# Optimization experiments

Measured on AMD Instinct MI355X. Metric: run time of the kernel, lower is better.

The kernel has to match this reference:

```python
import jax, jax.numpy as jnp
import numpy as np

ALPHA = 1.702
LIMIT = 7.0
EPS = 1e-5
TOP_K = 4


def setup_inputs() -> dict:
    key = jax.random.key(0)
    ks = jax.random.split(key, 8)
    B, S, H, I, E = 2, 512, 2048, 2048, 16
    return {
        "x": jax.random.normal(ks[0], (B, S, H), jnp.float32),
        "norm_w": jnp.ones((H,), jnp.float32),
        "gate_w": jax.random.normal(ks[1], (E, H), jnp.float32) * 0.02,
        "gate_b": jax.random.normal(ks[2], (E,), jnp.float32) * 0.02,
        "w1": jax.random.normal(ks[3], (E, 2 * I, H), jnp.float32) * 0.02,
        "b1": jax.random.normal(ks[4], (E, 2 * I), jnp.float32) * 0.02,
        "w2": jax.random.normal(ks[5], (E, H, I), jnp.float32) * 0.02,
        "b2": jax.random.normal(ks[6], (E, H), jnp.float32) * 0.02,
    }


def reference(x, norm_w, gate_w, gate_b, w1, b1, w2, b2):
    B, S, H = x.shape
    M = B * S
    E = gate_w.shape[0]
    xf = x.reshape(M, H)
    # RMSNorm
    t = xf * jax.lax.rsqrt(jnp.mean(xf * xf, axis=-1, keepdims=True) + EPS) * norm_w
    # Router: top-k over logits, then softmax over the selected k (sm_first=False)
    logits = t @ gate_w.T + gate_b  # [M, E]
    vals, idx = jax.lax.top_k(logits, TOP_K)
    gates_k = jax.nn.softmax(vals, axis=-1)  # [M, k]
    # Scatter top-k gate weights into dense [M, E] combine matrix
    G = jnp.zeros((M, E), x.dtype).at[jnp.arange(M)[:, None], idx].set(gates_k)
    # Expert MLP1 (all experts, combined sparsely below): [E, M, 2I]
    h = jnp.einsum('mh,eoh->emo', t, w1) + b1[:, None, :]
    # SwiGLU with clamp (gpt-oss): interleaved gate/linear columns
    a = jnp.minimum(h[..., ::2], LIMIT)
    b = jnp.clip(h[..., 1::2], -LIMIT, LIMIT)
    act = a * jax.nn.sigmoid(ALPHA * a) * (b + 1.0)  # [E, M, I]
    # Expert MLP2: [E, M, H]
    y = jnp.einsum('emi,edi->emd', act, w2) + b2[:, None, :]
    # Combine with gate weights (gammas scale full per-expert output incl. bias)
    delta = jnp.einsum('me,emd->md', G, y)
    return x + delta.reshape(B, S, H)
```

## Files before the change

kernel.cpp:

```cpp
#include <hip/hip_runtime.h>
#include <hip/hip_bf16.h>

constexpr int MTOK = 1024;
constexpr int HDIM = 2048;
constexpr int IDIM = 2048;
constexpr int NEXP = 16;
constexpr int TOPK = 4;
constexpr int NA   = MTOK * TOPK;

#define ALPHA_C 1.702f
#define LIMIT_C 7.0f
#define RMS_EPS 1e-5f

using short8 = __attribute__((ext_vector_type(8))) short;
using f32x4  = __attribute__((ext_vector_type(4))) float;

__device__ __forceinline__ unsigned short f2bf(float f) {
    unsigned u = __builtin_bit_cast(unsigned, f);
    u += 0x7fffu + ((u >> 16) & 1u);
    return (unsigned short)(u >> 16);
}

__device__ __forceinline__ unsigned pack2bf(float lo, float hi) {
    return (unsigned)f2bf(lo) | ((unsigned)f2bf(hi) << 16);
}

__device__ __forceinline__ short8 cvt8(const float4 a, const float4 b) {
    union { short8 s; unsigned u[4]; } r;
    r.u[0] = pack2bf(a.x, a.y);
    r.u[1] = pack2bf(a.z, a.w);
    r.u[2] = pack2bf(b.x, b.y);
    r.u[3] = pack2bf(b.z, b.w);
    return r.s;
}

__global__ __launch_bounds__(256) void k_router(
    const float* __restrict__ x, const float* __restrict__ norm_w,
    const float* __restrict__ gate_w, const float* __restrict__ gate_b,
    unsigned short* __restrict__ t_bf,
    int* __restrict__ counts, int* __restrict__ idx_of,
    int* __restrict__ slot_of, float* __restrict__ gate_mk)
{
    __shared__ float t_lds[HDIM];
    __shared__ float red[4];
    __shared__ float logits[NEXP];

    const int m   = blockIdx.x;
    const int tid = threadIdx.x;
    const float* xr = x + (size_t)m * HDIM;

    float4 v0 = ((const float4*)xr)[tid * 2];
    float4 v1 = ((const float4*)xr)[tid * 2 + 1];
    float ss = v0.x*v0.x + v0.y*v0.y + v0.z*v0.z + v0.w*v0.w
             + v1.x*v1.x + v1.y*v1.y + v1.z*v1.z + v1.w*v1.w;
    #pragma unroll
    for (int off = 32; off > 0; off >>= 1) ss += __shfl_down(ss, off);
    if ((tid & 63) == 0) red[tid >> 6] = ss;
    __syncthreads();
    float tot = red[0] + red[1] + red[2] + red[3];
    float scale = rsqrtf(tot / (float)HDIM + RMS_EPS);

    float4 n0 = ((const float4*)norm_w)[tid * 2];
    float4 n1 = ((const float4*)norm_w)[tid * 2 + 1];
    float t[8];
    t[0]=v0.x*scale*n0.x; t[1]=v0.y*scale*n0.y; t[2]=v0.z*scale*n0.z; t[3]=v0.w*scale*n0.w;
    t[4]=v1.x*scale*n1.x; t[5]=v1.y*scale*n1.y; t[6]=v1.z*scale*n1.z; t[7]=v1.w*scale*n1.w;
    short8 pk;
    #pragma unroll
    for (int j = 0; j < 8; ++j) {
        t_lds[tid * 8 + j] = t[j];
        pk[j] = (short)f2bf(t[j]);
    }
    *(short8*)(t_bf + (size_t)m * HDIM + tid * 8) = pk;
    __syncthreads();

    const int e = tid >> 4, j = tid & 15;
    const float4* gw4 = (const float4*)(gate_w + (size_t)e * HDIM);
    const float4* tl4 = (const float4*)t_lds;
    float part = 0.f;
    for (int h4 = j; h4 < HDIM / 4; h4 += 16) {
        float4 g = gw4[h4], tv = tl4[h4];
        part += g.x*tv.x + g.y*tv.y + g.z*tv.z + g.w*tv.w;
    }
    #pragma unroll
    for (int off = 8; off > 0; off >>= 1) part += __shfl_xor(part, off);
    if (j == 0) logits[e] = part + gate_b[e];
    __syncthreads();

    if (tid == 0) {
        float lv[NEXP];
        #pragma unroll
        for (int q = 0; q < NEXP; ++q) lv[q] = logits[q];
        int   sel[TOPK];
        float sv[TOPK];
        #pragma unroll
        for (int k = 0; k < TOPK; ++k) {
            float best = -1e30f; int bi = 0;
            for (int q = 0; q < NEXP; ++q)
                if (lv[q] > best) { best = lv[q]; bi = q; }
            sel[k] = bi; sv[k] = best; lv[bi] = -1e30f;
        }
        float mx = sv[0], s = 0.f, g[TOPK];
        #pragma unroll
        for (int k = 0; k < TOPK; ++k) { g[k] = __expf(sv[k] - mx); s += g[k]; }
        float inv = 1.f / s;
        #pragma unroll
        for (int k = 0; k < TOPK; ++k) {
            int a = m * TOPK + k;
            int slot = atomicAdd(&counts[sel[k]], 1);
            idx_of[a]  = sel[k];
            slot_of[a] = slot;
            gate_mk[a] = g[k] * inv;
        }
    }
}

__global__ void k_remap(const int* __restrict__ idx_of, const int* __restrict__ slot_of,
                        const int* __restrict__ counts,
                        int* __restrict__ token_of, int* __restrict__ rowidx)
{
    int a = blockIdx.x * blockDim.x + threadIdx.x;
    if (a >= NA) return;
    int e = idx_of[a];
    int off = 0;
    for (int q = 0; q < NEXP; ++q) off += (q < e) ? counts[q] : 0;
    int r = off + slot_of[a];
    token_of[r] = a >> 2;
    rowidx[a]   = r;
}

__global__ __launch_bounds__(256) void k_gemm1(
    const unsigned short* __restrict__ t_bf,
    const float* __restrict__ w1, const float* __restrict__ b1,
    const int* __restrict__ counts, const int* __restrict__ token_of,
    unsigned short* __restrict__ act)
{
    __shared__ unsigned char lB[2][2][5120];

    const int e = blockIdx.z;
    int ne = 0, roff = 0;
    #pragma unroll
    for (int q = 0; q < NEXP; ++q) {
        int cq = counts[q];
        roff += (q < e) ? cq : 0;
        ne    = (q == e) ? cq : ne;
    }
    const int brow = blockIdx.y * 320;
    if (brow >= ne) return;
    const int i0 = blockIdx.x * 32;
    const int tid = threadIdx.x;

    const int wv = tid >> 6, ln = tid & 63;
    const int lr = ln & 15, lk = ln >> 4;
    const int br = tid >> 2, bp = tid & 3;

    const unsigned short* aptr[5];
    #pragma unroll
    for (int mf = 0; mf < 5; ++mf) {
        int rg = brow + wv * 80 + mf * 16 + lr;
        int tok = token_of[roff + (rg < ne ? rg : 0)];
        aptr[mf] = t_bf + (size_t)tok * HDIM + lk * 8;
    }
    const int o = (br < 32) ? (2 * (i0 + br)) : (2 * (i0 + br - 32) + 1);
    const float* bsrc = w1 + ((size_t)e * (2 * IDIM) + o) * HDIM + bp * 16;

    float4 bS0[4], bS1[4], bS2[4], bS3[4];
    short8 aA0[5], aA1[5];
    f32x4  acc[5][4] = {};

    constexpr int NT = 32;

    {
        float4 p0 = *(const float4*)(bsrc);
        float4 p1 = *(const float4*)(bsrc + 4);
        float4 p2 = *(const float4*)(bsrc + 8);
        float4 p3 = *(const float4*)(bsrc + 12);
        *(short8*)(&lB[0][bp >> 1][br * 80 + (bp & 1) * 32])      = cvt8(p0, p1);
        *(short8*)(&lB[0][bp >> 1][br * 80 + (bp & 1) * 32 + 16]) = cvt8(p2, p3);
    }
    #pragma unroll
    for (int j = 0; j < 4; ++j) {
        bS1[j] = *(const float4*)(bsrc + 64  + j * 4);
        bS2[j] = *(const float4*)(bsrc + 128 + j * 4);
        bS3[j] = *(const float4*)(bsrc + 192 + j * 4);
    }
    #pragma unroll
    for (int mf = 0; mf < 5; ++mf) {
        aA0[mf] = *(const short8*)(aptr[mf]);
        aA1[mf] = *(const short8*)(aptr[mf] + 32);
    }
    asm volatile("s_waitcnt lgkmcnt(0)" ::: "memory");
    __builtin_amdgcn_s_barrier();

#define GSTEP(T_, SPUB, SISS)                                                            \
    {                                                                                    \
        const int t_ = (T_);                                                             \
        const int c_ = t_ & 1;                                                           \
        if (t_ + 1 < NT) {                                         \
            *(short8*)(&lB[c_ ^ 1][bp >> 1][br * 80 + (bp & 1) * 32])      =             \
                cvt8(SPUB[0], SPUB[1]);                                                  \
            *(short8*)(&lB[c_ ^ 1][bp >> 1][br * 80 + (bp & 1) * 32 + 16]) =             \
                cvt8(SPUB[2], SPUB[3]);                                                  \
        }                                                                                \
        if (t_ + 3 < NT) {                                           \
            _Pragma("unroll")                                                            \
            for (int j = 0; j < 4; ++j)                                                  \
                SISS[j] = *(const float4*)(bsrc + (t_ + 3) * 64 + j * 4);                \
        }                                                                                \
        short8 bfr[4];                                                                   \
        _Pragma("unroll")                                                                \
        for (int n = 0; n < 4; ++n)                                                      \
            bfr[n] = *(const short8*)(&lB[c_][0][(n * 16 + lr) * 80 + lk * 16]);         \
        _Pragma("unroll")                                                                \
        for (int mf = 0; mf < 5; ++mf)                                                   \
            _Pragma("unroll")                                                            \
            for (int n = 0; n < 4; ++n)                                                  \
                acc[mf][n] = __builtin_amdgcn_mfma_f32_16x16x32_bf16(                    \
                    aA0[mf], bfr[n], acc[mf][n], 0, 0, 0);                               \
        _Pragma("unroll")                                                                \
        for (int n = 0; n < 4; ++n)                                                      \
            bfr[n] = *(const short8*)(&lB[c_][1][(n * 16 + lr) * 80 + lk * 16]);         \
        _Pragma("unroll")                                                                \
        for (int mf = 0; mf < 5; ++mf)                                                   \
            _Pragma("unroll")                                                            \
            for (int n = 0; n < 4; ++n)                                                  \
                acc[mf][n] = __builtin_amdgcn_mfma_f32_16x16x32_bf16(                    \
                    aA1[mf], bfr[n], acc[mf][n], 0, 0, 0);                               \
        if (t_ + 1 < NT) {                           \
            _Pragma("unroll")                                                            \
            for (int mf = 0; mf < 5; ++mf) {                                             \
                aA0[mf] = *(const short8*)(aptr[mf] + (t_ + 1) * 64);                    \
                aA1[mf] = *(const short8*)(aptr[mf] + (t_ + 1) * 64 + 32);               \
            }                                                                            \
        }                                                                                \
        asm volatile("s_waitcnt lgkmcnt(0)" ::: "memory");                               \
        __builtin_amdgcn_s_barrier();                                                    \
    }

    for (int t8 = 0; t8 < NT / 4; ++t8) {
        const int tb = t8 * 4;
        GSTEP(tb + 0, bS1, bS3)
        GSTEP(tb + 1, bS2, bS0)
        GSTEP(tb + 2, bS3, bS1)
        GSTEP(tb + 3, bS0, bS2)
    }
#undef GSTEP

    #pragma unroll
    for (int n = 0; n < 2; ++n) {
        const int i = i0 + n * 16 + lr;
        const float ba = b1[(size_t)e * (2 * IDIM) + 2 * i];
        const float bb = b1[(size_t)e * (2 * IDIM) + 2 * i + 1];
        #pragma unroll
        for (int mf = 0; mf < 5; ++mf) {
            #pragma unroll
            for (int r = 0; r < 4; ++r) {
                const int rg = brow + wv * 80 + mf * 16 + lk * 4 + r;
                if (rg < ne) {
                    float ha = acc[mf][n][r] + ba;
                    float hb = acc[mf][n + 2][r] + bb;
                    float a = fminf(ha, LIMIT_C);
                    float b = fminf(fmaxf(hb, -LIMIT_C), LIMIT_C);
                    float s = 1.f / (1.f + __expf(-ALPHA_C * a));
                    act[(size_t)(roff + rg) * IDIM + i] = f2bf(a * s * (b + 1.f));
                }
            }
        }
    }
}

__global__ __launch_bounds__(256) void k_gemm2(
    const unsigned short* __restrict__ act,
    const float* __restrict__ w2, const float* __restrict__ b2,
    const int* __restrict__ counts, const int* __restrict__ token_of,
    unsigned short* __restrict__ ybuf)
{
    __shared__ unsigned char lB[2][2][5120];

    const int e = blockIdx.z;
    int ne = 0, roff = 0;
    #pragma unroll
    for (int q = 0; q < NEXP; ++q) {
        int cq = counts[q];
        roff += (q < e) ? cq : 0;
        ne    = (q == e) ? cq : ne;
    }
    const int brow = blockIdx.y * 320;
    if (brow >= ne) return;
    const int d0 = blockIdx.x * 64;
    const int tid = threadIdx.x;

    const int wv = tid >> 6, ln = tid & 63;
    const int lr = ln & 15, lk = ln >> 4;
    const int br = tid >> 2, bp = tid & 3;

    const unsigned short* aptr[5];
    #pragma unroll
    for (int mf = 0; mf < 5; ++mf) {
        int rg = brow + wv * 80 + mf * 16 + lr;
        int rc = (rg < ne) ? rg : 0;
        aptr[mf] = act + (size_t)(roff + rc) * IDIM + lk * 8;
    }
    const float* bsrc = w2 + ((size_t)e * HDIM + d0 + br) * IDIM + bp * 16;

    float4 bS0[4], bS1[4], bS2[4], bS3[4];
    short8 aA0[5], aA1[5];
    f32x4  acc[5][4] = {};

    constexpr int NT = 32;

    {
        float4 p0 = *(const float4*)(bsrc);
        float4 p1 = *(const float4*)(bsrc + 4);
        float4 p2 = *(const float4*)(bsrc + 8);
        float4 p3 = *(const float4*)(bsrc + 12);
        *(short8*)(&lB[0][bp >> 1][br * 80 + (bp & 1) * 32])      = cvt8(p0, p1);
        *(short8*)(&lB[0][bp >> 1][br * 80 + (bp & 1) * 32 + 16]) = cvt8(p2, p3);
    }
    #pragma unroll
    for (int j = 0; j < 4; ++j) {
        bS1[j] = *(const float4*)(bsrc + 64  + j * 4);
        bS2[j] = *(const float4*)(bsrc + 128 + j * 4);
        bS3[j] = *(const float4*)(bsrc + 192 + j * 4);
    }
    #pragma unroll
    for (int mf = 0; mf < 5; ++mf) {
        aA0[mf] = *(const short8*)(aptr[mf]);
        aA1[mf] = *(const short8*)(aptr[mf] + 32);
    }
    asm volatile("s_waitcnt lgkmcnt(0)" ::: "memory");
    __builtin_amdgcn_s_barrier();

#define GSTEP(T_, SPUB, SISS)                                                            \
    {                                                                                    \
        const int t_ = (T_);                                                             \
        const int c_ = t_ & 1;                                                           \
        if (t_ + 1 < NT) {                                                               \
            *(short8*)(&lB[c_ ^ 1][bp >> 1][br * 80 + (bp & 1) * 32])      =             \
                cvt8(SPUB[0], SPUB[1]);                                                  \
            *(short8*)(&lB[c_ ^ 1][bp >> 1][br * 80 + (bp & 1) * 32 + 16]) =             \
                cvt8(SPUB[2], SPUB[3]);                                                  \
        }                                                                                \
        if (t_ + 3 < NT) {                                                               \
            _Pragma("unroll")                                                            \
            for (int j = 0; j < 4; ++j)                                                  \
                SISS[j] = *(const float4*)(bsrc + (t_ + 3) * 64 + j * 4);                \
        }                                                                                \
        short8 bfr[4];                                                                   \
        _Pragma("unroll")                                                                \
        for (int n = 0; n < 4; ++n)                                                      \
            bfr[n] = *(const short8*)(&lB[c_][0][(n * 16 + lr) * 80 + lk * 16]);         \
        _Pragma("unroll")                                                                \
        for (int mf = 0; mf < 5; ++mf)                                                   \
            _Pragma("unroll")                                                            \
            for (int n = 0; n < 4; ++n)                                                  \
                acc[mf][n] = __builtin_amdgcn_mfma_f32_16x16x32_bf16(                    \
                    aA0[mf], bfr[n], acc[mf][n], 0, 0, 0);                               \
        _Pragma("unroll")                                                                \
        for (int n = 0; n < 4; ++n)                                                      \
            bfr[n] = *(const short8*)(&lB[c_][1][(n * 16 + lr) * 80 + lk * 16]);         \
        _Pragma("unroll")                                                                \
        for (int mf = 0; mf < 5; ++mf)                                                   \
            _Pragma("unroll")                                                            \
            for (int n = 0; n < 4; ++n)                                                  \
                acc[mf][n] = __builtin_amdgcn_mfma_f32_16x16x32_bf16(                    \
                    aA1[mf], bfr[n], acc[mf][n], 0, 0, 0);                               \
        if (t_ + 1 < NT) {                                                               \
            _Pragma("unroll")                                                            \
            for (int mf = 0; mf < 5; ++mf) {                                             \
                aA0[mf] = *(const short8*)(aptr[mf] + (t_ + 1) * 64);                    \
                aA1[mf] = *(const short8*)(aptr[mf] + (t_ + 1) * 64 + 32);               \
            }                                                                            \
        }                                                                                \
        asm volatile("s_waitcnt lgkmcnt(0)" ::: "memory");                               \
        __builtin_amdgcn_s_barrier();                                                    \
    }

    for (int t8 = 0; t8 < NT / 4; ++t8) {
        const int tb = t8 * 4;
        GSTEP(tb + 0, bS1, bS3)
        GSTEP(tb + 1, bS2, bS0)
        GSTEP(tb + 2, bS3, bS1)
        GSTEP(tb + 3, bS0, bS2)
    }
#undef GSTEP

    #pragma unroll
    for (int mf = 0; mf < 5; ++mf) {
        #pragma unroll
        for (int r = 0; r < 4; ++r) {
            const int rg = brow + wv * 80 + mf * 16 + lk * 4 + r;
            if (rg >= ne) continue;
            unsigned short* yrow = ybuf + (size_t)(roff + rg) * HDIM;
            #pragma unroll
            for (int n = 0; n < 4; ++n) {
                const int d = d0 + n * 16 + lr;
                yrow[d] = f2bf(acc[mf][n][r] + b2[(size_t)e * HDIM + d]);
            }
        }
    }
}

__global__ __launch_bounds__(256) void k_comb(
    const float* __restrict__ x, const unsigned short* __restrict__ ybuf,
    const int* __restrict__ rowidx, const float* __restrict__ gate_mk,
    float* __restrict__ out)
{
    __shared__ int   rws[TOPK];
    __shared__ float gws[TOPK];
    const int m = blockIdx.x;
    const int tid = threadIdx.x;
    if (tid < TOPK) {
        rws[tid] = rowidx[m * TOPK + tid];
        gws[tid] = gate_mk[m * TOPK + tid];
    }
    __syncthreads();
    const int d = tid * 8;
    float4 o0 = ((const float4*)(x + (size_t)m * HDIM + d))[0];
    float4 o1 = ((const float4*)(x + (size_t)m * HDIM + d))[1];
    #pragma unroll
    for (int k = 0; k < TOPK; ++k) {
        const float g = gws[k];
        short8 y = *(const short8*)(ybuf + (size_t)rws[k] * HDIM + d);
        float yv[8];
        #pragma unroll
        for (int j = 0; j < 8; ++j) {
            unsigned u = ((unsigned)(unsigned short)y[j]) << 16;
            yv[j] = __builtin_bit_cast(float, u);
        }
        o0.x += g * yv[0]; o0.y += g * yv[1]; o0.z += g * yv[2]; o0.w += g * yv[3];
        o1.x += g * yv[4]; o1.y += g * yv[5]; o1.z += g * yv[6]; o1.w += g * yv[7];
    }
    ((float4*)(out + (size_t)m * HDIM + d))[0] = o0;
    ((float4*)(out + (size_t)m * HDIM + d))[1] = o1;
}

extern "C" void kernel_launch(void* const* d_in, const int* in_sizes, int n_in,
                              void* d_out, int out_size, void* d_ws, size_t ws_size,
                              hipStream_t stream) {
    const float* x      = (const float*)d_in[0];
    const float* norm_w = (const float*)d_in[1];
    const float* gate_w = (const float*)d_in[2];
    const float* gate_b = (const float*)d_in[3];
    const float* w1     = (const float*)d_in[4];
    const float* b1     = (const float*)d_in[5];
    const float* w2     = (const float*)d_in[6];
    const float* b2     = (const float*)d_in[7];
    float* out = (float*)d_out;

    char* ws = (char*)d_ws;
    size_t off = 0;
    unsigned short* t_bf = (unsigned short*)(ws + off); off += (size_t)MTOK * HDIM * 2;
    unsigned short* actb = (unsigned short*)(ws + off); off += (size_t)NA * IDIM * 2;
    unsigned short* ybuf = (unsigned short*)(ws + off); off += (size_t)NA * HDIM * 2;
    int*   counts   = (int*)(ws + off);   off += 256;
    int*   idx_of   = (int*)(ws + off);   off += (size_t)NA * 4;
    int*   slot_of  = (int*)(ws + off);   off += (size_t)NA * 4;
    float* gate_mk  = (float*)(ws + off); off += (size_t)NA * 4;
    int*   token_of = (int*)(ws + off);   off += (size_t)NA * 4;
    int*   rowidx   = (int*)(ws + off);   off += (size_t)NA * 4;

    (void)hipMemsetAsync(counts, 0, 256, stream);
    k_router<<<MTOK, 256, 0, stream>>>(x, norm_w, gate_w, gate_b, t_bf,
                                       counts, idx_of, slot_of, gate_mk);
    k_remap<<<NA / 256, 256, 0, stream>>>(idx_of, slot_of, counts,
                                          token_of, rowidx);
    k_gemm1<<<dim3(IDIM / 32, (MTOK + 319) / 320, NEXP), 256, 0, stream>>>(
        t_bf, w1, b1, counts, token_of, actb);
    k_gemm2<<<dim3(HDIM / 64, (MTOK + 319) / 320, NEXP), 256, 0, stream>>>(
        actb, w2, b2, counts, token_of, ybuf);
    k_comb<<<MTOK, 256, 0, stream>>>(x, ybuf, rowidx, gate_mk, out);
}
```

Before: 428.4 us.

## Halve K-step in expert GEMMs to cut registers and target two blocks per CU

Both expert GEMM kernels move from 64-wide to 32-wide K steps (64 iterations instead of 32). This halves the staged B-fragment registers and the LDS tile, and the A fragments are now double-buffered in ping-pong register sets loaded one step ahead. Launch bounds now request two blocks per CU, and a sched_barrier pins global prefetches ahead of the LDS store and MFMA work. The aim is higher occupancy and better latency hiding, at the cost of twice as many barriers and smaller per-step MFMA batches.

```diff
diff --git a/kernel.cpp b/kernel.cpp
--- a/kernel.cpp
+++ b/kernel.cpp
@@ -129,13 +129,13 @@
     rowidx[a]   = r;
 }
 
-__global__ __launch_bounds__(256) void k_gemm1(
+__global__ __launch_bounds__(256, 2) void k_gemm1(
     const unsigned short* __restrict__ t_bf,
     const float* __restrict__ w1, const float* __restrict__ b1,
     const int* __restrict__ counts, const int* __restrict__ token_of,
     unsigned short* __restrict__ act)
 {
-    __shared__ unsigned char lB[2][2][5120];
+    __shared__ unsigned char lB[2][5120];
 
     const int e = blockIdx.z;
     int ne = 0, roff = 0;
@@ -162,87 +162,61 @@
         aptr[mf] = t_bf + (size_t)tok * HDIM + lk * 8;
     }
     const int o = (br < 32) ? (2 * (i0 + br)) : (2 * (i0 + br - 32) + 1);
-    const float* bsrc = w1 + ((size_t)e * (2 * IDIM) + o) * HDIM + bp * 16;
-
-    float4 bS0[4], bS1[4], bS2[4], bS3[4];
-    short8 aA0[5], aA1[5];
+    const float* bsrc = w1 + ((size_t)e * (2 * IDIM) + o) * HDIM + bp * 8;
+
+    short8 aE[5], aO[5];
+    float4 bS0[2], bS1[2], bS2[2], bS3[2];
     f32x4  acc[5][4] = {};
 
-    constexpr int NT = 32;
-
+    constexpr int NT = 64;
+
+    #pragma unroll
+    for (int mf = 0; mf < 5; ++mf) aE[mf] = *(const short8*)(aptr[mf]);
     {
         float4 p0 = *(const float4*)(bsrc);
         float4 p1 = *(const float4*)(bsrc + 4);
-        float4 p2 = *(const float4*)(bsrc + 8);
-        float4 p3 = *(const float4*)(bsrc + 12);
-        *(short8*)(&lB[0][bp >> 1][br * 80 + (bp & 1) * 32])      = cvt8(p0, p1);
-        *(short8*)(&lB[0][bp >> 1][br * 80 + (bp & 1) * 32 + 16]) = cvt8(p2, p3);
-    }
-    #pragma unroll
-    for (int j = 0; j < 4; ++j) {
-        bS1[j] = *(const float4*)(bsrc + 64  + j * 4);
-        bS2[j] = *(const float4*)(bsrc + 128 + j * 4);
-        bS3[j] = *(const float4*)(bsrc + 192 + j * 4);
-    }
-    #pragma unroll
-    for (int mf = 0; mf < 5; ++mf) {
-        aA0[mf] = *(const short8*)(aptr[mf]);
-        aA1[mf] = *(const short8*)(aptr[mf] + 32);
-    }
+        *(short8*)(&lB[0][br * 80 + bp * 16]) = cvt8(p0, p1);
+    }
+    bS1[0] = *(const float4*)(bsrc + 32);  bS1[1] = *(const float4*)(bsrc + 36);
+    bS2[0] = *(const float4*)(bsrc + 64);  bS2[1] = *(const float4*)(bsrc + 68);
     asm volatile("s_waitcnt lgkmcnt(0)" ::: "memory");
     __builtin_amdgcn_s_barrier();
 
-#define GSTEP(T_, SPUB, SISS)                                                            \
+#define GSTEP(T_, AU, AP, SPUB, SISS)                                                    \
     {                                                                                    \
         const int t_ = (T_);                                                             \
-        const int c_ = t_ & 1;                                                           \
-        if (t_ + 1 < NT) {                                         \
-            *(short8*)(&lB[c_ ^ 1][bp >> 1][br * 80 + (bp & 1) * 32])      =             \
-                cvt8(SPUB[0], SPUB[1]);                                                  \
-            *(short8*)(&lB[c_ ^ 1][bp >> 1][br * 80 + (bp & 1) * 32 + 16]) =             \
-                cvt8(SPUB[2], SPUB[3]);                                                  \
+        if (t_ + 1 < NT) {                                          \
+            _Pragma("unroll")                                                            \
+            for (int mf = 0; mf < 5; ++mf)                                               \
+                AP[mf] = *(const short8*)(aptr[mf] + (t_ + 1) * 32);                     \
         }                                                                                \
-        if (t_ + 3 < NT) {                                           \
-            _Pragma("unroll")                                                            \
-            for (int j = 0; j < 4; ++j)                                                  \
-                SISS[j] = *(const float4*)(bsrc + (t_ + 3) * 64 + j * 4);                \
+        if (t_ + 3 < NT) {                                         \
+            SISS[0] = *(const float4*)(bsrc + (t_ + 3) * 32);                            \
+            SISS[1] = *(const float4*)(bsrc + (t_ + 3) * 32 + 4);                        \
         }                                                                                \
-        short8 bfr[4];                                                                   \
+        __builtin_amdgcn_sched_barrier(0);                      \
+        if (t_ + 1 < NT)                                          \
+            *(short8*)(&lB[(t_ + 1) & 1][br * 80 + bp * 16]) = cvt8(SPUB[0], SPUB[1]);   \
+        short8 bfr[4];                                            \
         _Pragma("unroll")                                                                \
         for (int n = 0; n < 4; ++n)                                                      \
-            bfr[n] = *(const short8*)(&lB[c_][0][(n * 16 + lr) * 80 + lk * 16]);         \
+            bfr[n] = *(const short8*)(&lB[t_ & 1][(n * 16 + lr) * 80 + lk * 16]);        \
         _Pragma("unroll")                                                                \
         for (int mf = 0; mf < 5; ++mf)                                                   \
             _Pragma("unroll")                                                            \
             for (int n = 0; n < 4; ++n)                                                  \
                 acc[mf][n] = __builtin_amdgcn_mfma_f32_16x16x32_bf16(                    \
-                    aA0[mf], bfr[n], acc[mf][n], 0, 0, 0);                               \
-        _Pragma("unroll")                                                                \
-        for (int n = 0; n < 4; ++n)                                                      \
-            bfr[n] = *(const short8*)(&lB[c_][1][(n * 16 + lr) * 80 + lk * 16]);         \
-        _Pragma("unroll")                                                                \
-        for (int mf = 0; mf < 5; ++mf)                                                   \
-            _Pragma("unroll")                                                            \
-            for (int n = 0; n < 4; ++n)                                                  \
-                acc[mf][n] = __builtin_amdgcn_mfma_f32_16x16x32_bf16(                    \
-                    aA1[mf], bfr[n], acc[mf][n], 0, 0, 0);                               \
-        if (t_ + 1 < NT) {                           \
-            _Pragma("unroll")                                                            \
-            for (int mf = 0; mf < 5; ++mf) {                                             \
-                aA0[mf] = *(const short8*)(aptr[mf] + (t_ + 1) * 64);                    \
-                aA1[mf] = *(const short8*)(aptr[mf] + (t_ + 1) * 64 + 32);               \
-            }                                                                            \
-        }                                                                                \
+                    AU[mf], bfr[n], acc[mf][n], 0, 0, 0);                                \
         asm volatile("s_waitcnt lgkmcnt(0)" ::: "memory");                               \
         __builtin_amdgcn_s_barrier();                                                    \
     }
 
-    for (int t8 = 0; t8 < NT / 4; ++t8) {
-        const int tb = t8 * 4;
-        GSTEP(tb + 0, bS1, bS3)
-        GSTEP(tb + 1, bS2, bS0)
-        GSTEP(tb + 2, bS3, bS1)
-        GSTEP(tb + 3, bS0, bS2)
+    for (int t4 = 0; t4 < NT / 4; ++t4) {
+        const int tb = t4 * 4;
+        GSTEP(tb + 0, aE, aO, bS1, bS3)
+        GSTEP(tb + 1, aO, aE, bS2, bS0)
+        GSTEP(tb + 2, aE, aO, bS3, bS1)
+        GSTEP(tb + 3, aO, aE, bS0, bS2)
     }
 #undef GSTEP
 
@@ -269,13 +243,13 @@
     }
 }
 
-__global__ __launch_bounds__(256) void k_gemm2(
+__global__ __launch_bounds__(256, 2) void k_gemm2(
     const unsigned short* __restrict__ act,
     const float* __restrict__ w2, const float* __restrict__ b2,
     const int* __restrict__ counts, const int* __restrict__ token_of,
     unsigned short* __restrict__ ybuf)
 {
-    __shared__ unsigned char lB[2][2][5120];
+    __shared__ unsigned char lB[2][5120];
 
     const int e = blockIdx.z;
     int ne = 0, roff = 0;
@@ -301,87 +275,61 @@
         int rc = (rg < ne) ? rg : 0;
         aptr[mf] = act + (size_t)(roff + rc) * IDIM + lk * 8;
     }
-    const float* bsrc = w2 + ((size_t)e * HDIM + d0 + br) * IDIM + bp * 16;
-
-    float4 bS0[4], bS1[4], bS2[4], bS3[4];
-    short8 aA0[5], aA1[5];
+    const float* bsrc = w2 + ((size_t)e * HDIM + d0 + br) * IDIM + bp * 8;
+
+    short8 aE[5], aO[5];
+    float4 bS0[2], bS1[2], bS2[2], bS3[2];
     f32x4  acc[5][4] = {};
 
-    constexpr int NT = 32;
-
+    constexpr int NT = 64;
+
+    #pragma unroll
+    for (int mf = 0; mf < 5; ++mf) aE[mf] = *(const short8*)(aptr[mf]);
     {
         float4 p0 = *(const float4*)(bsrc);
         float4 p1 = *(const float4*)(bsrc + 4);
-        float4 p2 = *(const float4*)(bsrc + 8);
-        float4 p3 = *(const float4*)(bsrc + 12);
-        *(short8*)(&lB[0][bp >> 1][br * 80 + (bp & 1) * 32])      = cvt8(p0, p1);
-        *(short8*)(&lB[0][bp >> 1][br * 80 + (bp & 1) * 32 + 16]) = cvt8(p2, p3);
-    }
-    #pragma unroll
-    for (int j = 0; j < 4; ++j) {
-        bS1[j] = *(const float4*)(bsrc + 64  + j * 4);
-        bS2[j] = *(const float4*)(bsrc + 128 + j * 4);
-        bS3[j] = *(const float4*)(bsrc + 192 + j * 4);
-    }
-    #pragma unroll
-    for (int mf = 0; mf < 5; ++mf) {
-        aA0[mf] = *(const short8*)(aptr[mf]);
-        aA1[mf] = *(const short8*)(aptr[mf] + 32);
-    }
+        *(short8*)(&lB[0][br * 80 + bp * 16]) = cvt8(p0, p1);
+    }
+    bS1[0] = *(const float4*)(bsrc + 32);  bS1[1] = *(const float4*)(bsrc + 36);
+    bS2[0] = *(const float4*)(bsrc + 64);  bS2[1] = *(const float4*)(bsrc + 68);
     asm volatile("s_waitcnt lgkmcnt(0)" ::: "memory");
     __builtin_amdgcn_s_barrier();
 
-#define GSTEP(T_, SPUB, SISS)                                                            \
+#define GSTEP(T_, AU, AP, SPUB, SISS)                                                    \
     {                                                                                    \
         const int t_ = (T_);                                                             \
-        const int c_ = t_ & 1;                                                           \
         if (t_ + 1 < NT) {                                                               \
-            *(short8*)(&lB[c_ ^ 1][bp >> 1][br * 80 + (bp & 1) * 32])      =             \
-                cvt8(SPUB[0], SPUB[1]);                                                  \
-            *(short8*)(&lB[c_ ^ 1][bp >> 1][br * 80 + (bp & 1) * 32 + 16]) =             \
-                cvt8(SPUB[2], SPUB[3]);                                                  \
+            _Pragma("unroll")                                                            \
+            for (int mf = 0; mf < 5; ++mf)                                               \
+                AP[mf] = *(const short8*)(aptr[mf] + (t_ + 1) * 32);                     \
         }                                                                                \
         if (t_ + 3 < NT) {                                                               \
-            _Pragma("unroll")                                                            \
-            for (int j = 0; j < 4; ++j)                                                  \
-                SISS[j] = *(const float4*)(bsrc + (t_ + 3) * 64 + j * 4);                \
+            SISS[0] = *(const float4*)(bsrc + (t_ + 3) * 32);                            \
+            SISS[1] = *(const float4*)(bsrc + (t_ + 3) * 32 + 4);                        \
         }                                                                                \
+        __builtin_amdgcn_sched_barrier(0);                                               \
+        if (t_ + 1 < NT)                                                                 \
+            *(short8*)(&lB[(t_ + 1) & 1][br * 80 + bp * 16]) = cvt8(SPUB[0], SPUB[1]);   \
         short8 bfr[4];                                                                   \
         _Pragma("unroll")                                                                \
         for (int n = 0; n < 4; ++n)                                                      \
-            bfr[n] = *(const short8*)(&lB[c_][0][(n * 16 + lr) * 80 + lk * 16]);         \
+            bfr[n] = *(const short8*)(&lB[t_ & 1][(n * 16 + lr) * 80 + lk * 16]);        \
         _Pragma("unroll")                                                                \
         for (int mf = 0; mf < 5; ++mf)                                                   \
             _Pragma("unroll")                                                            \
             for (int n = 0; n < 4; ++n)                                                  \
                 acc[mf][n] = __builtin_amdgcn_mfma_f32_16x16x32_bf16(                    \
-                    aA0[mf], bfr[n], acc[mf][n], 0, 0, 0);                               \
-        _Pragma("unroll")                                                                \
-        for (int n = 0; n < 4; ++n)                                                      \
-            bfr[n] = *(const short8*)(&lB[c_][1][(n * 16 + lr) * 80 + lk * 16]);         \
-        _Pragma("unroll")                                                                \
-        for (int mf = 0; mf < 5; ++mf)                                                   \
-            _Pragma("unroll")                                                            \
-            for (int n = 0; n < 4; ++n)                                                  \
-                acc[mf][n] = __builtin_amdgcn_mfma_f32_16x16x32_bf16(                    \
-                    aA1[mf], bfr[n], acc[mf][n], 0, 0, 0);                               \
-        if (t_ + 1 < NT) {                                                               \
-            _Pragma("unroll")                                                            \
-            for (int mf = 0; mf < 5; ++mf) {                                             \
-                aA0[mf] = *(const short8*)(aptr[mf] + (t_ + 1) * 64);                    \
-                aA1[mf] = *(const short8*)(aptr[mf] + (t_ + 1) * 64 + 32);               \
-            }                                                                            \
-        }                                                                                \
+                    AU[mf], bfr[n], acc[mf][n], 0, 0, 0);                                \
         asm volatile("s_waitcnt lgkmcnt(0)" ::: "memory");                               \
         __builtin_amdgcn_s_barrier();                                                    \
     }
 
-    for (int t8 = 0; t8 < NT / 4; ++t8) {
-        const int tb = t8 * 4;
-        GSTEP(tb + 0, bS1, bS3)
-        GSTEP(tb + 1, bS2, bS0)
-        GSTEP(tb + 2, bS3, bS1)
-        GSTEP(tb + 3, bS0, bS2)
+    for (int t4 = 0; t4 < NT / 4; ++t4) {
+        const int tb = t4 * 4;
+        GSTEP(tb + 0, aE, aO, bS1, bS3)
+        GSTEP(tb + 1, aO, aE, bS2, bS0)
+        GSTEP(tb + 2, aE, aO, bS3, bS1)
+        GSTEP(tb + 3, aO, aE, bS0, bS2)
     }
 #undef GSTEP
 
```

New measurement: 410.9 us. 4.1% less time.
